# Performance work log

Hardware: AMD Instinct MI355X
Metric: run time of the kernel (lower is better)

## Reference

```python
import jax, jax.numpy as jnp
import numpy as np

B, L, N, S, M = 4096, 512, 12, 128, 12


def setup_inputs() -> dict:
    key = jax.random.key(0)
    ks = jax.random.split(key, 8)
    sc = 1.0 / np.sqrt(S)
    scn = 1.0 / np.sqrt(N)
    return {
        "x": jax.random.normal(ks[0], (B, L, N), dtype=jnp.float32),
        "a0": jax.random.uniform(ks[1], (B, S), dtype=jnp.float32),
        "U_w": jax.random.uniform(ks[2], (N, S), minval=-scn, maxval=scn, dtype=jnp.float32),
        "U_b": jax.random.uniform(ks[3], (S,), minval=-scn, maxval=scn, dtype=jnp.float32),
        "W_w": jax.random.uniform(ks[4], (S, S), minval=-sc, maxval=sc, dtype=jnp.float32),
        "W_b": jax.random.uniform(ks[5], (S,), minval=-sc, maxval=sc, dtype=jnp.float32),
        "V_w": jax.random.uniform(ks[6], (S, M), minval=-sc, maxval=sc, dtype=jnp.float32),
        "V_b": jax.random.uniform(ks[7], (M,), minval=-sc, maxval=sc, dtype=jnp.float32),
    }


def reference(x, a0, U_w, U_b, W_w, W_b, V_w, V_b):
    # Elman RNN cell: a_t = relu(U(x_t) + W(a_{t-1})); output y = V(a_L)
    # Precompute input projection for all steps at once: [B,L,S]
    ux = jnp.einsum("bln,ns->bls", x, U_w) + U_b

    def step(a, ux_t):  # a: [B,S], ux_t: [B,S]
        a_new = jax.nn.relu(ux_t + a @ W_w + W_b)
        return a_new, None

    a_last, _ = jax.lax.scan(step, a0, jnp.swapaxes(ux, 0, 1))  # scan over L
    return a_last @ V_w + V_b  # [B, M]
```

## Files before the change

### kernel.cpp

```cpp
#include <hip/hip_runtime.h>
#include <hip/hip_bf16.h>

typedef __attribute__((ext_vector_type(8))) short bf16x8;
typedef __attribute__((ext_vector_type(4))) float f32x4;

#define L_SEQ 512
#define N_IN 12
#define S_DIM 128
#define M_OUT 12
#define LPAD 40
#define KT_STRIDE (16*LPAD)

__device__ inline short f2bf(float f) {
    union { float f; unsigned u; } q; q.f = f;
    unsigned r = (q.u + 0x7fffu + ((q.u >> 16) & 1u)) >> 16;
    return (short)r;
}
__device__ inline unsigned cvtpk(float lo, float hi) {
    unsigned r;
    asm("v_cvt_pk_bf16_f32 %0, %1, %2" : "=v"(r) : "v"(lo), "v"(hi));
    return r;
}
__device__ inline int s_perm(int kt, int q, int j) {
    return 32 * kt + 16 * (j >> 2) + 4 * q + (j & 3);
}
__device__ inline void block_sync() {
    asm volatile("s_waitcnt lgkmcnt(0)" ::: "memory");
    __builtin_amdgcn_s_barrier();
}

__global__ __launch_bounds__(512, 1)
void elman_kernel(const float* __restrict__ x,
                  const float* __restrict__ a0,
                  const float* __restrict__ U_w,
                  const float* __restrict__ U_b,
                  const float* __restrict__ W_w,
                  const float* __restrict__ W_b,
                  const float* __restrict__ V_w,
                  const float* __restrict__ V_b,
                  float* __restrict__ out)
{
    __shared__ __align__(16) short stx[2][4 * KT_STRIDE];
    __shared__ __align__(16) short xr[4][64 * 8];

    const int tid  = threadIdx.x;
    const int w    = tid >> 6;
    const int l    = tid & 63;
    const int n    = l & 15;
    const int q    = l >> 4;
    const bool qodd = (q & 1);
    const int b0   = blockIdx.x * 16;
    const int row  = b0 + n;
    const int fragoff = n * LPAD + q * 8;
    const int h    = w & 3;

    const float* xpA = x + (size_t)row * L_SEQ * N_IN + (q & 1) * 8;
    const float* xpB = xpA + (qodd ? 0 : 4);

#define MAKE_XF(XF, XA, XB) do {                                                       \
    union { unsigned uu[4]; bf16x8 v; } xu_;                                           \
    xu_.uu[0] = cvtpk(XA.x, XA.y);                                                     \
    xu_.uu[1] = cvtpk(XA.z, XA.w);                                                     \
    xu_.uu[2] = qodd ? 0x00003F80u : cvtpk(XB.x, XB.y);        \
    xu_.uu[3] = qodd ? 0u          : cvtpk(XB.z, XB.w);                                \
    XF = xu_.v;                                                                        \
} while (0)

    bf16x8 wf[2][4]; bf16x8 uf[2];
    if (w < 4) {
        #pragma unroll
        for (int hh = 0; hh < 2; ++hh) {
            const int c = (2 * w + hh) * 16 + n;
            #pragma unroll
            for (int li = 0; li < 4; ++li) {
                const int kt = (w + li) & 3;
                #pragma unroll
                for (int j = 0; j < 8; ++j)
                    wf[hh][li][j] = f2bf(W_w[(size_t)s_perm(kt, q, j) * S_DIM + c]);
            }
            #pragma unroll
            for (int j = 0; j < 8; ++j) {
                const int k = q * 8 + j;
                float v;
                if (k < N_IN)       v = U_w[(size_t)k * S_DIM + c];
                else if (k == N_IN) v = W_b[c] + U_b[c];
                else                v = 0.f;
                uf[hh][j] = f2bf(v);
            }
        }
    }

    for (int idx = tid; idx < 4 * 16 * 32; idx += 512) {
        const int kt = idx >> 9, r = (idx >> 5) & 15, qj = idx & 31;
        const int s = s_perm(kt, qj >> 3, qj & 7);
        stx[0][kt * KT_STRIDE + r * LPAD + qj] = f2bf(a0[(size_t)(b0 + r) * S_DIM + s]);
    }

    float4 pA, pB;
    if (w >= 4) {
        if (h < 3) {
            float4 sa = *(const float4*)(xpA + (size_t)h * N_IN);
            float4 sb = *(const float4*)(xpB + (size_t)h * N_IN);
            bf16x8 xf; MAKE_XF(xf, sa, sb);
            *(bf16x8*)&xr[h][l * 8] = xf;
        }
        const int t0 = (h == 3) ? 3 : (h + 4);
        pA = *(const float4*)(xpA + (size_t)t0 * N_IN);
        pB = *(const float4*)(xpB + (size_t)t0 * N_IN);
    }
    block_sync();

    bf16x8 stOwnR, stf1, stf2, stf3, xfc_cur, xfc_next;
    f32x4 accU0, accU1, c0a, c1a;
    if (w < 4) {
        const short* rd = &stx[0][0];
        stOwnR = *(const bf16x8*)&rd[((w + 0) & 3) * KT_STRIDE + fragoff];
        stf1   = *(const bf16x8*)&rd[((w + 1) & 3) * KT_STRIDE + fragoff];
        stf2   = *(const bf16x8*)&rd[((w + 2) & 3) * KT_STRIDE + fragoff];
        stf3   = *(const bf16x8*)&rd[((w + 3) & 3) * KT_STRIDE + fragoff];
        bf16x8 xf0 = *(const bf16x8*)&xr[0][l * 8];
        xfc_cur    = *(const bf16x8*)&xr[1][l * 8];
        xfc_next   = *(const bf16x8*)&xr[2][l * 8];
        f32x4 z = {0.f, 0.f, 0.f, 0.f};
        accU0 = __builtin_amdgcn_mfma_f32_16x16x32_bf16(uf[0], xf0, z, 0, 0, 0);
        accU1 = __builtin_amdgcn_mfma_f32_16x16x32_bf16(uf[1], xf0, z, 0, 0, 0);
        c0a = __builtin_amdgcn_mfma_f32_16x16x32_bf16(wf[0][0], stOwnR, accU0, 0, 0, 0);
        c1a = __builtin_amdgcn_mfma_f32_16x16x32_bf16(wf[1][0], stOwnR, accU1, 0, 0, 0);
    }

#define STEP(UU) do {                                                                  \
    const int tt = t + (UU);                                                           \
    if (w < 4) {                                                                       \
        __builtin_amdgcn_s_setprio(1);                                                 \
        f32x4 z = {0.f, 0.f, 0.f, 0.f};                                                \
                   \
        accU0 = __builtin_amdgcn_mfma_f32_16x16x32_bf16(uf[0], xfc_cur, z, 0, 0, 0);   \
        accU1 = __builtin_amdgcn_mfma_f32_16x16x32_bf16(uf[1], xfc_cur, z, 0, 0, 0);   \
                                                                   \
        c0a = __builtin_amdgcn_mfma_f32_16x16x32_bf16(wf[0][1], stf1, c0a, 0, 0, 0);   \
        c1a = __builtin_amdgcn_mfma_f32_16x16x32_bf16(wf[1][1], stf1, c1a, 0, 0, 0);   \
        f32x4 c0b = __builtin_amdgcn_mfma_f32_16x16x32_bf16(wf[0][2], stf2, z, 0, 0, 0); \
        f32x4 c1b = __builtin_amdgcn_mfma_f32_16x16x32_bf16(wf[1][2], stf2, z, 0, 0, 0); \
        c0b = __builtin_amdgcn_mfma_f32_16x16x32_bf16(wf[0][3], stf3, c0b, 0, 0, 0);   \
        c1b = __builtin_amdgcn_mfma_f32_16x16x32_bf16(wf[1][3], stf3, c1b, 0, 0, 0);   \
                                                                 \
        union { unsigned uu[4]; bf16x8 v; } su;                                        \
        su.uu[0] = cvtpk(fmaxf(c0a[0] + c0b[0], 0.f), fmaxf(c0a[1] + c0b[1], 0.f));    \
        su.uu[1] = cvtpk(fmaxf(c0a[2] + c0b[2], 0.f), fmaxf(c0a[3] + c0b[3], 0.f));    \
        su.uu[2] = cvtpk(fmaxf(c1a[0] + c1b[0], 0.f), fmaxf(c1a[1] + c1b[1], 0.f));    \
        su.uu[3] = cvtpk(fmaxf(c1a[2] + c1b[2], 0.f), fmaxf(c1a[3] + c1b[3], 0.f));    \
        stOwnR = su.v;                                                                 \
                 \
        c0a = __builtin_amdgcn_mfma_f32_16x16x32_bf16(wf[0][0], stOwnR, accU0, 0, 0, 0); \
        c1a = __builtin_amdgcn_mfma_f32_16x16x32_bf16(wf[1][0], stOwnR, accU1, 0, 0, 0); \
        *(bf16x8*)&stx[(tt + 1) & 1][w * KT_STRIDE + fragoff] = stOwnR;                \
        xfc_cur = xfc_next;                                                            \
        __builtin_amdgcn_s_setprio(0);                                                 \
    } else {                                                                           \
                   \
        if (h == (((UU) + 3) & 3)) {                                                   \
            bf16x8 xf_; MAKE_XF(xf_, pA, pB);                                          \
            *(bf16x8*)&xr[h][l * 8] = xf_;                                             \
            const int s2_ = (tt + 7 < L_SEQ) ? (tt + 7) : (L_SEQ - 1);                 \
            pA = *(const float4*)(xpA + (size_t)s2_ * N_IN);                           \
            pB = *(const float4*)(xpB + (size_t)s2_ * N_IN);                           \
        }                                                                              \
    }                                                                                  \
    block_sync();                                                                      \
    if (w < 4) {                                                                       \
        const short* rd_ = &stx[(tt + 1) & 1][0];                                      \
        stf1 = *(const bf16x8*)&rd_[((w + 1) & 3) * KT_STRIDE + fragoff];              \
        stf2 = *(const bf16x8*)&rd_[((w + 2) & 3) * KT_STRIDE + fragoff];              \
        stf3 = *(const bf16x8*)&rd_[((w + 3) & 3) * KT_STRIDE + fragoff];              \
        xfc_next = *(const bf16x8*)&xr[(((UU) + 3) & 3)][l * 8];         \
    }                                                                                  \
} while (0)

    for (int t = 0; t < L_SEQ; t += 4) {
        STEP(0);
        STEP(1);
        STEP(2);
        STEP(3);
    }
#undef STEP
#undef MAKE_XF

    if (w == 0) {
        f32x4 acc = {0.f, 0.f, 0.f, 0.f};
        #pragma unroll
        for (int li = 0; li < 4; ++li) {
            bf16x8 vf;
            #pragma unroll
            for (int j = 0; j < 8; ++j)
                vf[j] = (n < M_OUT)
                      ? f2bf(V_w[(size_t)s_perm(li, q, j) * M_OUT + n])
                      : (short)0;
            const bf16x8 stt = (li == 0) ? stOwnR : (li == 1) ? stf1 : (li == 2) ? stf2 : stf3;
            acc = __builtin_amdgcn_mfma_f32_16x16x32_bf16(vf, stt, acc, 0, 0, 0);
        }
        #pragma unroll
        for (int j = 0; j < 4; ++j) {
            const int m = 4 * q + j;
            if (m < M_OUT)
                out[(size_t)row * M_OUT + m] = acc[j] + V_b[m];
        }
    }
}

extern "C" void kernel_launch(void* const* d_in, const int* in_sizes, int n_in,
                              void* d_out, int out_size, void* d_ws, size_t ws_size,
                              hipStream_t stream) {
    const float* x   = (const float*)d_in[0];
    const float* a0  = (const float*)d_in[1];
    const float* U_w = (const float*)d_in[2];
    const float* U_b = (const float*)d_in[3];
    const float* W_w = (const float*)d_in[4];
    const float* W_b = (const float*)d_in[5];
    const float* V_w = (const float*)d_in[6];
    const float* V_b = (const float*)d_in[7];
    float* out = (float*)d_out;

    hipLaunchKernelGGL(elman_kernel, dim3(4096 / 16), dim3(512), 0, stream,
                       x, a0, U_w, U_b, W_w, W_b, V_w, V_b, out);
}
```

Before: 117.6 us.

## Process two interleaved 16-row batch tiles per block to hide recurrence latency

Each block now handles 32 batch rows as two independent 16-row tiles, interleaving their recurrence MFMAs within each step so one tile's dependent chain can overlap the other's. The per-step MFMA chain is also restructured into four independent products summed at the end, with the input projection folded into the last one. This halves the grid to 128 blocks, which may leave compute units idle. It also doubles the per-wave work between barriers.

```diff
diff --git a/kernel.cpp b/kernel.cpp
--- a/kernel.cpp
+++ b/kernel.cpp
@@ -40,8 +40,8 @@
                   const float* __restrict__ V_b,
                   float* __restrict__ out)
 {
-    __shared__ __align__(16) short stx[2][4 * KT_STRIDE];
-    __shared__ __align__(16) short xr[4][64 * 8];
+    __shared__ __align__(16) short stx[2][2][4 * KT_STRIDE];
+    __shared__ __align__(16) short xr[2][4][64 * 8];
 
     const int tid  = threadIdx.x;
     const int w    = tid >> 6;
@@ -49,13 +49,14 @@
     const int n    = l & 15;
     const int q    = l >> 4;
     const bool qodd = (q & 1);
-    const int b0   = blockIdx.x * 16;
-    const int row  = b0 + n;
+    const int b0   = blockIdx.x * 32;
     const int fragoff = n * LPAD + q * 8;
     const int h    = w & 3;
 
-    const float* xpA = x + (size_t)row * L_SEQ * N_IN + (q & 1) * 8;
-    const float* xpB = xpA + (qodd ? 0 : 4);
+    const float* xp0_lo = x + (size_t)(b0 + n) * L_SEQ * N_IN + (q & 1) * 8;
+    const float* xp0_hi = xp0_lo + (qodd ? 0 : 4);
+    const float* xp1_lo = x + (size_t)(b0 + 16 + n) * L_SEQ * N_IN + (q & 1) * 8;
+    const float* xp1_hi = xp1_lo + (qodd ? 0 : 4);
 
 #define MAKE_XF(XF, XA, XB) do {                                                       \
     union { unsigned uu[4]; bf16x8 v; } xu_;                                           \
@@ -90,89 +91,117 @@
         }
     }
 
-    for (int idx = tid; idx < 4 * 16 * 32; idx += 512) {
-        const int kt = idx >> 9, r = (idx >> 5) & 15, qj = idx & 31;
+    for (int idx = tid; idx < 2 * 4 * 16 * 32; idx += 512) {
+        const int ti = idx >> 11, rem = idx & 2047;
+        const int kt = rem >> 9, r = (rem >> 5) & 15, qj = rem & 31;
         const int s = s_perm(kt, qj >> 3, qj & 7);
-        stx[0][kt * KT_STRIDE + r * LPAD + qj] = f2bf(a0[(size_t)(b0 + r) * S_DIM + s]);
-    }
-
-    float4 pA, pB;
+        stx[ti][0][kt * KT_STRIDE + r * LPAD + qj] =
+            f2bf(a0[(size_t)(b0 + ti * 16 + r) * S_DIM + s]);
+    }
+
+    float4 p0A, p0B, p1A, p1B;
     if (w >= 4) {
         if (h < 3) {
-            float4 sa = *(const float4*)(xpA + (size_t)h * N_IN);
-            float4 sb = *(const float4*)(xpB + (size_t)h * N_IN);
+            float4 sa = *(const float4*)(xp0_lo + (size_t)h * N_IN);
+            float4 sb = *(const float4*)(xp0_hi + (size_t)h * N_IN);
             bf16x8 xf; MAKE_XF(xf, sa, sb);
-            *(bf16x8*)&xr[h][l * 8] = xf;
+            *(bf16x8*)&xr[0][h][l * 8] = xf;
+            sa = *(const float4*)(xp1_lo + (size_t)h * N_IN);
+            sb = *(const float4*)(xp1_hi + (size_t)h * N_IN);
+            MAKE_XF(xf, sa, sb);
+            *(bf16x8*)&xr[1][h][l * 8] = xf;
         }
         const int t0 = (h == 3) ? 3 : (h + 4);
-        pA = *(const float4*)(xpA + (size_t)t0 * N_IN);
-        pB = *(const float4*)(xpB + (size_t)t0 * N_IN);
+        p0A = *(const float4*)(xp0_lo + (size_t)t0 * N_IN);
+        p0B = *(const float4*)(xp0_hi + (size_t)t0 * N_IN);
+        p1A = *(const float4*)(xp1_lo + (size_t)t0 * N_IN);
+        p1B = *(const float4*)(xp1_hi + (size_t)t0 * N_IN);
     }
     block_sync();
 
-    bf16x8 stOwnR, stf1, stf2, stf3, xfc_cur, xfc_next;
-    f32x4 accU0, accU1, c0a, c1a;
+    bf16x8 st0Own, st0f1, st0f2, st0f3, xfc0_cur, xfc0_next;
+    bf16x8 st1Own, st1f1, st1f2, st1f3, xfc1_cur, xfc1_next;
+    f32x4 aU00, aU01, aU10, aU11;
     if (w < 4) {
-        const short* rd = &stx[0][0];
-        stOwnR = *(const bf16x8*)&rd[((w + 0) & 3) * KT_STRIDE + fragoff];
-        stf1   = *(const bf16x8*)&rd[((w + 1) & 3) * KT_STRIDE + fragoff];
-        stf2   = *(const bf16x8*)&rd[((w + 2) & 3) * KT_STRIDE + fragoff];
-        stf3   = *(const bf16x8*)&rd[((w + 3) & 3) * KT_STRIDE + fragoff];
-        bf16x8 xf0 = *(const bf16x8*)&xr[0][l * 8];
-        xfc_cur    = *(const bf16x8*)&xr[1][l * 8];
-        xfc_next   = *(const bf16x8*)&xr[2][l * 8];
+        const short* rd0 = &stx[0][0][0];
+        st0Own = *(const bf16x8*)&rd0[((w + 0) & 3) * KT_STRIDE + fragoff];
+        st0f1  = *(const bf16x8*)&rd0[((w + 1) & 3) * KT_STRIDE + fragoff];
+        st0f2  = *(const bf16x8*)&rd0[((w + 2) & 3) * KT_STRIDE + fragoff];
+        st0f3  = *(const bf16x8*)&rd0[((w + 3) & 3) * KT_STRIDE + fragoff];
+        const short* rd1 = &stx[1][0][0];
+        st1Own = *(const bf16x8*)&rd1[((w + 0) & 3) * KT_STRIDE + fragoff];
+        st1f1  = *(const bf16x8*)&rd1[((w + 1) & 3) * KT_STRIDE + fragoff];
+        st1f2  = *(const bf16x8*)&rd1[((w + 2) & 3) * KT_STRIDE + fragoff];
+        st1f3  = *(const bf16x8*)&rd1[((w + 3) & 3) * KT_STRIDE + fragoff];
+        bf16x8 xf00 = *(const bf16x8*)&xr[0][0][l * 8];
+        xfc0_cur    = *(const bf16x8*)&xr[0][1][l * 8];
+        xfc0_next   = *(const bf16x8*)&xr[0][2][l * 8];
+        bf16x8 xf10 = *(const bf16x8*)&xr[1][0][l * 8];
+        xfc1_cur    = *(const bf16x8*)&xr[1][1][l * 8];
+        xfc1_next   = *(const bf16x8*)&xr[1][2][l * 8];
         f32x4 z = {0.f, 0.f, 0.f, 0.f};
-        accU0 = __builtin_amdgcn_mfma_f32_16x16x32_bf16(uf[0], xf0, z, 0, 0, 0);
-        accU1 = __builtin_amdgcn_mfma_f32_16x16x32_bf16(uf[1], xf0, z, 0, 0, 0);
-        c0a = __builtin_amdgcn_mfma_f32_16x16x32_bf16(wf[0][0], stOwnR, accU0, 0, 0, 0);
-        c1a = __builtin_amdgcn_mfma_f32_16x16x32_bf16(wf[1][0], stOwnR, accU1, 0, 0, 0);
-    }
+        aU00 = __builtin_amdgcn_mfma_f32_16x16x32_bf16(uf[0], xf00, z, 0, 0, 0);
+        aU01 = __builtin_amdgcn_mfma_f32_16x16x32_bf16(uf[1], xf00, z, 0, 0, 0);
+        aU10 = __builtin_amdgcn_mfma_f32_16x16x32_bf16(uf[0], xf10, z, 0, 0, 0);
+        aU11 = __builtin_amdgcn_mfma_f32_16x16x32_bf16(uf[1], xf10, z, 0, 0, 0);
+    }
+
+#define BODY(TI, STOWN, STF1, STF2, STF3, XCUR, XNEXT, AU0, AU1, TT) do {              \
+    f32x4 z_ = {0.f, 0.f, 0.f, 0.f};                                                   \
+    f32x4 nU0 = __builtin_amdgcn_mfma_f32_16x16x32_bf16(uf[0], XCUR, z_, 0, 0, 0);     \
+    f32x4 nU1 = __builtin_amdgcn_mfma_f32_16x16x32_bf16(uf[1], XCUR, z_, 0, 0, 0);     \
+    f32x4 c00 = __builtin_amdgcn_mfma_f32_16x16x32_bf16(wf[0][0], STOWN, z_, 0, 0, 0); \
+    f32x4 c10 = __builtin_amdgcn_mfma_f32_16x16x32_bf16(wf[1][0], STOWN, z_, 0, 0, 0); \
+    f32x4 c01 = __builtin_amdgcn_mfma_f32_16x16x32_bf16(wf[0][1], STF1, z_, 0, 0, 0);  \
+    f32x4 c11 = __builtin_amdgcn_mfma_f32_16x16x32_bf16(wf[1][1], STF1, z_, 0, 0, 0);  \
+    f32x4 c02 = __builtin_amdgcn_mfma_f32_16x16x32_bf16(wf[0][2], STF2, z_, 0, 0, 0);  \
+    f32x4 c12 = __builtin_amdgcn_mfma_f32_16x16x32_bf16(wf[1][2], STF2, z_, 0, 0, 0);  \
+    f32x4 c03 = __builtin_amdgcn_mfma_f32_16x16x32_bf16(wf[0][3], STF3, AU0, 0, 0, 0); \
+    f32x4 c13 = __builtin_amdgcn_mfma_f32_16x16x32_bf16(wf[1][3], STF3, AU1, 0, 0, 0); \
+    AU0 = nU0; AU1 = nU1;                                                              \
+    f32x4 s0 = (c00 + c01) + (c02 + c03);                                              \
+    f32x4 s1 = (c10 + c11) + (c12 + c13);                                              \
+    union { unsigned uu[4]; bf16x8 v; } su;                                            \
+    su.uu[0] = cvtpk(fmaxf(s0[0], 0.f), fmaxf(s0[1], 0.f));                            \
+    su.uu[1] = cvtpk(fmaxf(s0[2], 0.f), fmaxf(s0[3], 0.f));                            \
+    su.uu[2] = cvtpk(fmaxf(s1[0], 0.f), fmaxf(s1[1], 0.f));                            \
+    su.uu[3] = cvtpk(fmaxf(s1[2], 0.f), fmaxf(s1[3], 0.f));                            \
+    STOWN = su.v;                                                                      \
+    *(bf16x8*)&stx[TI][((TT) + 1) & 1][w * KT_STRIDE + fragoff] = STOWN;               \
+    XCUR = XNEXT;                                                                      \
+} while (0)
 
 #define STEP(UU) do {                                                                  \
     const int tt = t + (UU);                                                           \
     if (w < 4) {                                                                       \
         __builtin_amdgcn_s_setprio(1);                                                 \
-        f32x4 z = {0.f, 0.f, 0.f, 0.f};                                                \
-                   \
-        accU0 = __builtin_amdgcn_mfma_f32_16x16x32_bf16(uf[0], xfc_cur, z, 0, 0, 0);   \
-        accU1 = __builtin_amdgcn_mfma_f32_16x16x32_bf16(uf[1], xfc_cur, z, 0, 0, 0);   \
-                                                                   \
-        c0a = __builtin_amdgcn_mfma_f32_16x16x32_bf16(wf[0][1], stf1, c0a, 0, 0, 0);   \
-        c1a = __builtin_amdgcn_mfma_f32_16x16x32_bf16(wf[1][1], stf1, c1a, 0, 0, 0);   \
-        f32x4 c0b = __builtin_amdgcn_mfma_f32_16x16x32_bf16(wf[0][2], stf2, z, 0, 0, 0); \
-        f32x4 c1b = __builtin_amdgcn_mfma_f32_16x16x32_bf16(wf[1][2], stf2, z, 0, 0, 0); \
-        c0b = __builtin_amdgcn_mfma_f32_16x16x32_bf16(wf[0][3], stf3, c0b, 0, 0, 0);   \
-        c1b = __builtin_amdgcn_mfma_f32_16x16x32_bf16(wf[1][3], stf3, c1b, 0, 0, 0);   \
-                                                                 \
-        union { unsigned uu[4]; bf16x8 v; } su;                                        \
-        su.uu[0] = cvtpk(fmaxf(c0a[0] + c0b[0], 0.f), fmaxf(c0a[1] + c0b[1], 0.f));    \
-        su.uu[1] = cvtpk(fmaxf(c0a[2] + c0b[2], 0.f), fmaxf(c0a[3] + c0b[3], 0.f));    \
-        su.uu[2] = cvtpk(fmaxf(c1a[0] + c1b[0], 0.f), fmaxf(c1a[1] + c1b[1], 0.f));    \
-        su.uu[3] = cvtpk(fmaxf(c1a[2] + c1b[2], 0.f), fmaxf(c1a[3] + c1b[3], 0.f));    \
-        stOwnR = su.v;                                                                 \
-                 \
-        c0a = __builtin_amdgcn_mfma_f32_16x16x32_bf16(wf[0][0], stOwnR, accU0, 0, 0, 0); \
-        c1a = __builtin_amdgcn_mfma_f32_16x16x32_bf16(wf[1][0], stOwnR, accU1, 0, 0, 0); \
-        *(bf16x8*)&stx[(tt + 1) & 1][w * KT_STRIDE + fragoff] = stOwnR;                \
-        xfc_cur = xfc_next;                                                            \
+        BODY(0, st0Own, st0f1, st0f2, st0f3, xfc0_cur, xfc0_next, aU00, aU01, tt);     \
+        BODY(1, st1Own, st1f1, st1f2, st1f3, xfc1_cur, xfc1_next, aU10, aU11, tt);     \
         __builtin_amdgcn_s_setprio(0);                                                 \
-    } else {                                                                           \
-                   \
-        if (h == (((UU) + 3) & 3)) {                                                   \
-            bf16x8 xf_; MAKE_XF(xf_, pA, pB);                                          \
-            *(bf16x8*)&xr[h][l * 8] = xf_;                                             \
-            const int s2_ = (tt + 7 < L_SEQ) ? (tt + 7) : (L_SEQ - 1);                 \
-            pA = *(const float4*)(xpA + (size_t)s2_ * N_IN);                           \
-            pB = *(const float4*)(xpB + (size_t)s2_ * N_IN);                           \
-        }                                                                              \
+    } else if (h == (((UU) + 3) & 3)) {                                                \
+        bf16x8 xf_;                                                                    \
+        MAKE_XF(xf_, p0A, p0B);                                                        \
+        *(bf16x8*)&xr[0][h][l * 8] = xf_;                                              \
+        MAKE_XF(xf_, p1A, p1B);                                                        \
+        *(bf16x8*)&xr[1][h][l * 8] = xf_;                                              \
+        const int s2_ = (tt + 7 < L_SEQ) ? (tt + 7) : (L_SEQ - 1);                     \
+        p0A = *(const float4*)(xp0_lo + (size_t)s2_ * N_IN);                           \
+        p0B = *(const float4*)(xp0_hi + (size_t)s2_ * N_IN);                           \
+        p1A = *(const float4*)(xp1_lo + (size_t)s2_ * N_IN);                           \
+        p1B = *(const float4*)(xp1_hi + (size_t)s2_ * N_IN);                           \
     }                                                                                  \
     block_sync();                                                                      \
     if (w < 4) {                                                                       \
-        const short* rd_ = &stx[(tt + 1) & 1][0];                                      \
-        stf1 = *(const bf16x8*)&rd_[((w + 1) & 3) * KT_STRIDE + fragoff];              \
-        stf2 = *(const bf16x8*)&rd_[((w + 2) & 3) * KT_STRIDE + fragoff];              \
-        stf3 = *(const bf16x8*)&rd_[((w + 3) & 3) * KT_STRIDE + fragoff];              \
-        xfc_next = *(const bf16x8*)&xr[(((UU) + 3) & 3)][l * 8];         \
+        const short* rd0_ = &stx[0][(tt + 1) & 1][0];                                  \
+        st0f1 = *(const bf16x8*)&rd0_[((w + 1) & 3) * KT_STRIDE + fragoff];            \
+        st0f2 = *(const bf16x8*)&rd0_[((w + 2) & 3) * KT_STRIDE + fragoff];            \
+        st0f3 = *(const bf16x8*)&rd0_[((w + 3) & 3) * KT_STRIDE + fragoff];            \
+        const short* rd1_ = &stx[1][(tt + 1) & 1][0];                                  \
+        st1f1 = *(const bf16x8*)&rd1_[((w + 1) & 3) * KT_STRIDE + fragoff];            \
+        st1f2 = *(const bf16x8*)&rd1_[((w + 2) & 3) * KT_STRIDE + fragoff];            \
+        st1f3 = *(const bf16x8*)&rd1_[((w + 3) & 3) * KT_STRIDE + fragoff];            \
+        xfc0_next = *(const bf16x8*)&xr[0][(((UU) + 3) & 3)][l * 8];                   \
+        xfc1_next = *(const bf16x8*)&xr[1][(((UU) + 3) & 3)][l * 8];                   \
     }                                                                                  \
 } while (0)
 
@@ -183,26 +212,32 @@
         STEP(3);
     }
 #undef STEP
+#undef BODY
 #undef MAKE_XF
 
-    if (w == 0) {
+    if (w < 2) {
+        const bf16x8 fr0 = (w == 0) ? st0Own : st1Own;
+        const bf16x8 fr1 = (w == 0) ? st0f1  : st1f1;
+        const bf16x8 fr2 = (w == 0) ? st0f2  : st1f2;
+        const bf16x8 fr3 = (w == 0) ? st0f3  : st1f3;
         f32x4 acc = {0.f, 0.f, 0.f, 0.f};
         #pragma unroll
         for (int li = 0; li < 4; ++li) {
+            const int kt = (w + li) & 3;
             bf16x8 vf;
             #pragma unroll
             for (int j = 0; j < 8; ++j)
                 vf[j] = (n < M_OUT)
-                      ? f2bf(V_w[(size_t)s_perm(li, q, j) * M_OUT + n])
+                      ? f2bf(V_w[(size_t)s_perm(kt, q, j) * M_OUT + n])
                       : (short)0;
-            const bf16x8 stt = (li == 0) ? stOwnR : (li == 1) ? stf1 : (li == 2) ? stf2 : stf3;
+            const bf16x8 stt = (li == 0) ? fr0 : (li == 1) ? fr1 : (li == 2) ? fr2 : fr3;
             acc = __builtin_amdgcn_mfma_f32_16x16x32_bf16(vf, stt, acc, 0, 0, 0);
         }
         #pragma unroll
         for (int j = 0; j < 4; ++j) {
             const int m = 4 * q + j;
             if (m < M_OUT)
-                out[(size_t)row * M_OUT + m] = acc[j] + V_b[m];
+                out[(size_t)(b0 + w * 16 + n) * M_OUT + m] = acc[j] + V_b[m];
         }
     }
 }
@@ -220,6 +255,6 @@
     const float* V_b = (const float*)d_in[7];
     float* out = (float*)d_out;
 
-    hipLaunchKernelGGL(elman_kernel, dim3(4096 / 16), dim3(512), 0, stream,
+    hipLaunchKernelGGL(elman_kernel, dim3(4096 / 32), dim3(512), 0, stream,
                        x, a0, U_w, U_b, W_w, W_b, V_w, V_b, out);
 }
```

Result: slower. 213.7 us (+81.7%).
